# Kernel optimization log

Hardware: AMD Instinct MI355X
Metric: run time of the kernel (lower is better)

Reference implementation:

```python
import jax, jax.numpy as jnp
import numpy as np

R, N, F, H, C = 3, 100000, 256, 128, 2
N0, S1, D1, S2, D2 = 16384, 16384, 4096, 4096, 512


def setup_inputs() -> dict:
    key = jax.random.key(0)
    ks = jax.random.split(key, 13)
    return {
        "features": jax.random.normal(ks[0], (N, F), jnp.float32),
        "src_nodes": jax.random.randint(ks[1], (R, N0), 0, N),
        "dstsrc2src1": jax.random.randint(ks[2], (R, S1), 0, N0),
        "dstsrc2dst1": jax.random.randint(ks[3], (R, D1), 0, N0),
        "dif_mat1": jax.random.uniform(ks[4], (R, D1, S1), jnp.float32) / S1,
        "dstsrc2src2": jax.random.randint(ks[5], (R, S2), 0, D1),
        "dstsrc2dst2": jax.random.randint(ks[6], (R, D2), 0, D1),
        "dif_mat2": jax.random.uniform(ks[7], (R, D2, S2), jnp.float32) / S2,
        "w1": jax.random.normal(ks[8], (2 * F, H), jnp.float32) * 0.05,
        "w2": jax.random.normal(ks[9], (2 * H, H), jnp.float32) * 0.05,
        "relation_vectors": jax.random.uniform(ks[10], (R, H), jnp.float32),
        "attention_vec": jax.random.uniform(ks[11], (2 * H, 1), jnp.float32),
        "classifier_w": jax.random.normal(ks[12], (H, C), jnp.float32) * 0.05,
    }


def _agg(x, d2s, d2d, dif, w, rel_vec, att_vec):
    # x: [n, din]; dif: [d, s]; w: [2*din, H]
    agg = dif @ x[d2s]                                  # mean-diffused neighbor feats [d, din]
    h = jnp.concatenate([agg, x[d2d]], axis=1) @ w      # [d, H]
    rel = jnp.broadcast_to(rel_vec[None, :], (h.shape[0], rel_vec.shape[0]))
    score = (jnp.concatenate([h, rel], axis=1) @ att_vec)[:, 0]  # [d]
    att = jax.nn.softmax(score)                         # softmax over batch nodes
    return h * att[:, None]


def reference(features, src_nodes, dstsrc2src1, dstsrc2dst1, dif_mat1,
              dstsrc2src2, dstsrc2dst2, dif_mat2, w1, w2,
              relation_vectors, attention_vec, classifier_w):
    def per_relation(src, s1, d1, m1, s2, d2, m2, rel_vec):
        x = features[src]                               # gather node feats [N0, F]
        x = _agg(x, s1, d1, m1, w1, rel_vec, attention_vec)   # [D1, H]
        x = _agg(x, s2, d2, m2, w2, rel_vec, attention_vec)   # [D2, H]
        return x

    xs = jax.vmap(per_relation)(src_nodes, dstsrc2src1, dstsrc2dst1, dif_mat1,
                                dstsrc2src2, dstsrc2dst2, dif_mat2, relation_vectors)
    summed = jnp.sum(xs, axis=0)                        # sum over relations [D2, H]
    inv_norm = jax.lax.rsqrt(jnp.maximum(jnp.sum(summed * summed, axis=1, keepdims=True), 1e-12))
    normed = summed * inv_norm                          # tf.nn.l2_normalize(axis=1)
    return jax.nn.softmax(normed @ classifier_w, axis=-1)
```

## Files before the change

### kernel.cpp

```cpp
#include <hip/hip_runtime.h>
#include <hip/hip_bf16.h>
#include <math.h>

constexpr int Rc  = 3;
constexpr int Fc  = 256;
constexpr int Hc  = 128;
constexpr int N0c = 16384;
constexpr int S1c = 16384;
constexpr int D1c = 4096;
constexpr int S2c = 4096;
constexpr int D2c = 512;
constexpr int KH1 = 4;
constexpr int KH2 = 16;

typedef __bf16 bf16x8 __attribute__((ext_vector_type(8)));
typedef float  f32x4  __attribute__((ext_vector_type(4)));

__device__ __forceinline__ void glds16(const void* g, void* l) {
  __builtin_amdgcn_global_load_lds(
      (const __attribute__((address_space(1))) void*)g,
      (__attribute__((address_space(3))) void*)l, 16, 0, 0);
}

__device__ __forceinline__ bf16x8 cvt2(const float4 a, const float4 b) {
  bf16x8 c;
  c[0] = (__bf16)a.x; c[1] = (__bf16)a.y; c[2] = (__bf16)a.z; c[3] = (__bf16)a.w;
  c[4] = (__bf16)b.x; c[5] = (__bf16)b.y; c[6] = (__bf16)b.z; c[7] = (__bf16)b.w;
  return c;
}

__device__ __forceinline__ unsigned short bfbits(float v) {
  __bf16 b = (__bf16)v; unsigned short u;
  __builtin_memcpy(&u, &b, 2); return u;
}

__global__ __launch_bounds__(256, 2)
void wpack(const float* __restrict__ w1, const float* __restrict__ w2,
           unsigned char* __restrict__ wp) {
  const int tile = blockIdx.x, half = blockIdx.y, t = threadIdx.x;
  const float* src; int row0;
  if (tile < 4)       { src = w1; row0 = tile * 64; }
  else if (tile < 8)  { src = w1; row0 = 256 + (tile - 4) * 64; }
  else if (tile < 10) { src = w2; row0 = (tile - 8) * 64; }
  else                { src = w2; row0 = 128 + (tile - 10) * 64; }
  unsigned char* dst = wp + ((size_t)half * 12 + tile) * 16384;
  __shared__ float sm[64][132];
  {
    const int r = t >> 2, c0 = (t & 3) * 32;
#pragma unroll
    for (int j = 0; j < 8; j++)
      *(float4*)&sm[r][c0 + 4 * j] = *(const float4*)(src + (size_t)(row0 + r) * 128 + c0 + 4 * j);
  }
  __syncthreads();
  if (t < 128) {
    const int n = t;
#pragma unroll
    for (int ch = 0; ch < 8; ch++) {
      bf16x8 o;
#pragma unroll
      for (int e = 0; e < 8; e++) {
        float v = sm[ch * 8 + e][n];
        __bf16 h = (__bf16)v;
        o[e] = half ? (__bf16)(v - (float)h) : h;
      }
      *(bf16x8*)(dst + n * 128 + ((ch ^ (n & 7)) * 16)) = o;
    }
  }
}

__global__ __launch_bounds__(256, 3)
void gemm_gather(const float* __restrict__ Abase, int astride,
                 const int* __restrict__ srcn, const int* __restrict__ idx,
                 const float* __restrict__ scl,
                 const unsigned char* __restrict__ Bh,
                 const unsigned char* __restrict__ Bl,
                 float* __restrict__ Cf, unsigned char* __restrict__ Cp,
                 int rows, int K) {
  const int rel = blockIdx.y, s0 = blockIdx.x * 64;
  const int t = threadIdx.x, lane = t & 63, w = t >> 6;
  const int NT = K >> 6;
  const int mh = w >> 1, nh = w & 1;

  __shared__ __bf16 Asm[64 * 64];
  __shared__ __bf16 Bhs[128 * 64];
  __shared__ __bf16 Bls[128 * 64];

  const int arow = t >> 2, ak0 = (t & 3) * 16;
  const int row = s0 + arow;
  size_t arowg;
  if (idx) arowg = (size_t)srcn[rel * N0c + idx[(size_t)rel * rows + row]];
  else     arowg = (size_t)rel * rows + row;
  const float* aptr = Abase + arowg * astride + ak0;
  const float sc = scl ? scl[(size_t)rel * rows + row] : 1.0f;
  const int ac0 = ak0 >> 3;
  __bf16* asw0 = &Asm[arow * 64 + ((ac0    ) ^ (arow & 7)) * 8];
  __bf16* asw1 = &Asm[arow * 64 + ((ac0 + 1) ^ (arow & 7)) * 8];

  f32x4 acc[2][4] = {};

  for (int tl = 0; tl < NT; ++tl) {
    asm volatile("s_waitcnt lgkmcnt(0)" ::: "memory");
    __builtin_amdgcn_s_barrier();
    __builtin_amdgcn_sched_barrier(0);
    {
      const unsigned char* bh = Bh + (size_t)tl * 16384 + w * 4096 + lane * 16;
      const unsigned char* bl = Bl + (size_t)tl * 16384 + w * 4096 + lane * 16;
      char* dh = (char*)Bhs + w * 4096;
      char* dl = (char*)Bls + w * 4096;
#pragma unroll
      for (int i = 0; i < 4; i++) glds16(bh + i * 1024, dh + i * 1024);
#pragma unroll
      for (int i = 0; i < 4; i++) glds16(bl + i * 1024, dl + i * 1024);
    }
    {
      float4 a[4];
#pragma unroll
      for (int j = 0; j < 4; j++) a[j] = *(const float4*)(aptr + tl * 64 + 4 * j);
      if (scl) {
#pragma unroll
        for (int j = 0; j < 4; j++) { a[j].x *= sc; a[j].y *= sc; a[j].z *= sc; a[j].w *= sc; }
      }
      *(bf16x8*)asw0 = cvt2(a[0], a[1]);
      *(bf16x8*)asw1 = cvt2(a[2], a[3]);
    }
    asm volatile("s_waitcnt vmcnt(0) lgkmcnt(0)" ::: "memory");
    __builtin_amdgcn_s_barrier();
    __builtin_amdgcn_sched_barrier(0);
#pragma unroll
    for (int ks = 0; ks < 2; ks++) {
      const int ch = ks * 4 + (lane >> 4);
      bf16x8 af[2], bh[4], bl[4];
#pragma unroll
      for (int mi = 0; mi < 2; mi++) {
        int r = mh * 32 + mi * 16 + (lane & 15);
        af[mi] = *(const bf16x8*)&Asm[r * 64 + ((ch ^ (r & 7)) * 8)];
      }
#pragma unroll
      for (int ni = 0; ni < 4; ni++) {
        int n = nh * 64 + ni * 16 + (lane & 15);
        bh[ni] = *(const bf16x8*)&Bhs[n * 64 + ((ch ^ (n & 7)) * 8)];
        bl[ni] = *(const bf16x8*)&Bls[n * 64 + ((ch ^ (n & 7)) * 8)];
      }
#pragma unroll
      for (int mi = 0; mi < 2; mi++)
#pragma unroll
        for (int ni = 0; ni < 4; ni++) {
          acc[mi][ni] = __builtin_amdgcn_mfma_f32_16x16x32_bf16(af[mi], bh[ni], acc[mi][ni], 0, 0, 0);
          acc[mi][ni] = __builtin_amdgcn_mfma_f32_16x16x32_bf16(af[mi], bl[ni], acc[mi][ni], 0, 0, 0);
        }
    }
  }
  if (Cf) {
#pragma unroll
    for (int mi = 0; mi < 2; mi++)
#pragma unroll
      for (int ni = 0; ni < 4; ni++) {
        const int col = nh * 64 + ni * 16 + (lane & 15);
#pragma unroll
        for (int j = 0; j < 4; j++) {
          const int r = mh * 32 + mi * 16 + (lane >> 4) * 4 + j;
          Cf[((size_t)rel * rows + s0 + r) * 128 + col] = acc[mi][ni][j];
        }
      }
  } else {
    unsigned char* tile = Cp + ((size_t)(rel * (rows >> 6) + blockIdx.x)) * 16384;
#pragma unroll
    for (int mi = 0; mi < 2; mi++)
#pragma unroll
      for (int ni = 0; ni < 4; ni++) {
        const int sl0 = mh * 32 + mi * 16 + (lane >> 4) * 4;
        const int n = nh * 64 + ni * 16 + (lane & 15);
        const int ch = sl0 >> 3, e0 = sl0 & 7, cs = ch ^ (n & 7);
        ushort4 u;
        u.x = bfbits(acc[mi][ni][0]); u.y = bfbits(acc[mi][ni][1]);
        u.z = bfbits(acc[mi][ni][2]); u.w = bfbits(acc[mi][ni][3]);
        *(ushort4*)(tile + n * 128 + cs * 16 + e0 * 2) = u;
      }
  }
}

__global__ __launch_bounds__(256, 3)
void gemm_big(const float* __restrict__ A, const unsigned char* __restrict__ Bp,
              float* __restrict__ C, int M, int KTOT) {
  const int rel = blockIdx.z, kh = blockIdx.y;
  const int m0 = blockIdx.x * 64;
  const int t = threadIdx.x, lane = t & 63, w = t >> 6;
  const int KB = KTOT / gridDim.y, NT = KB >> 6;
  const int mh = w >> 1, nh = w & 1;

  const float* Ag = A + ((size_t)rel * M + m0) * KTOT + (size_t)kh * KB;
  const unsigned char* Bt = Bp + ((size_t)rel * (KTOT >> 6) + (size_t)kh * NT) * 16384;
  float* Cg = C + (((size_t)kh * Rc + rel) * M + m0) * 128;

  __shared__ __bf16 Asm[64 * 64];
  __shared__ __bf16 Bsm[2][128 * 64];

  f32x4 acc[2][4] = {};
  const int arow = t >> 2, ak0 = (t & 3) * 16;
  const float* aptr = Ag + (size_t)arow * KTOT + ak0;
  const int ac0 = ak0 >> 3;
  __bf16* asw0 = &Asm[arow * 64 + ((ac0    ) ^ (arow & 7)) * 8];
  __bf16* asw1 = &Asm[arow * 64 + ((ac0 + 1) ^ (arow & 7)) * 8];
  const unsigned char* bsrc = Bt + w * 4096 + lane * 16;

  float4 a0[4], a1[4];
#pragma unroll
  for (int j = 0; j < 4; j++) a0[j] = *(const float4*)(aptr + 4 * j);
  {
    char* bd = (char*)Bsm[0] + w * 4096;
#pragma unroll
    for (int i = 0; i < 4; i++) glds16(bsrc + i * 1024, bd + i * 1024);
  }

  for (int tl = 0; tl < NT; ++tl) {
    const int cur = tl & 1;
    asm volatile("s_waitcnt lgkmcnt(0)" ::: "memory");
    __builtin_amdgcn_s_barrier();
    __builtin_amdgcn_sched_barrier(0);
    if (tl + 1 < NT) {
      const unsigned char* bs = bsrc + (size_t)(tl + 1) * 16384;
      char* bd = (char*)Bsm[cur ^ 1] + w * 4096;
#pragma unroll
      for (int i = 0; i < 4; i++) glds16(bs + i * 1024, bd + i * 1024);
      const float* ap = aptr + (size_t)(tl + 1) * 64;
#pragma unroll
      for (int j = 0; j < 4; j++) a1[j] = *(const float4*)(ap + 4 * j);
    }
    *(bf16x8*)asw0 = cvt2(a0[0], a0[1]);
    *(bf16x8*)asw1 = cvt2(a0[2], a0[3]);
    if (tl + 1 < NT)
      asm volatile("s_waitcnt vmcnt(8) lgkmcnt(0)" ::: "memory");
    else
      asm volatile("s_waitcnt vmcnt(0) lgkmcnt(0)" ::: "memory");
    __builtin_amdgcn_s_barrier();
    __builtin_amdgcn_sched_barrier(0);
    const __bf16* Bc = Bsm[cur];
#pragma unroll
    for (int ks = 0; ks < 2; ks++) {
      const int ch = ks * 4 + (lane >> 4);
      bf16x8 af[2], bfr[4];
#pragma unroll
      for (int mi = 0; mi < 2; mi++) {
        int r = mh * 32 + mi * 16 + (lane & 15);
        af[mi] = *(const bf16x8*)&Asm[r * 64 + ((ch ^ (r & 7)) * 8)];
      }
#pragma unroll
      for (int ni = 0; ni < 4; ni++) {
        int n = nh * 64 + ni * 16 + (lane & 15);
        bfr[ni] = *(const bf16x8*)&Bc[n * 64 + ((ch ^ (n & 7)) * 8)];
      }
#pragma unroll
      for (int mi = 0; mi < 2; mi++)
#pragma unroll
        for (int ni = 0; ni < 4; ni++)
          acc[mi][ni] = __builtin_amdgcn_mfma_f32_16x16x32_bf16(af[mi], bfr[ni], acc[mi][ni], 0, 0, 0);
    }
#pragma unroll
    for (int j = 0; j < 4; j++) a0[j] = a1[j];
  }
#pragma unroll
  for (int mi = 0; mi < 2; mi++)
#pragma unroll
    for (int ni = 0; ni < 4; ni++) {
      const int col = nh * 64 + ni * 16 + (lane & 15);
#pragma unroll
      for (int j = 0; j < 4; j++) {
        const int r = mh * 32 + mi * 16 + (lane >> 4) * 4 + j;
        Cg[(size_t)r * 128 + col] = acc[mi][ni][j];
      }
    }
}

__global__ __launch_bounds__(256, 2)
void pgpack(const float* __restrict__ P, const int* __restrict__ d2s2,
            unsigned char* __restrict__ PGp) {
  const int rel = blockIdx.y, kb = blockIdx.x, t = threadIdx.x;
  __shared__ __bf16 sm[64][136];
  {
    const int kl = t >> 2, c0 = (t & 3) * 32;
    const int sr = d2s2[rel * S2c + kb * 64 + kl];
    const float4* p = (const float4*)(P + ((size_t)rel * D1c + sr) * 128 + c0);
#pragma unroll
    for (int j = 0; j < 4; j++)
      *(bf16x8*)&sm[kl][c0 + 8 * j] = cvt2(p[2 * j], p[2 * j + 1]);
  }
  __syncthreads();
  if (t < 128) {
    const int n = t;
    unsigned char* dst = PGp + ((size_t)(rel * (S2c >> 6) + kb)) * 16384;
#pragma unroll
    for (int ch = 0; ch < 8; ch++) {
      bf16x8 o;
#pragma unroll
      for (int e = 0; e < 8; e++) o[e] = sm[ch * 8 + e][n];
      *(bf16x8*)(dst + n * 128 + ((ch ^ (n & 7)) * 16)) = o;
    }
  }
}

__global__ __launch_bounds__(128, 4)
void combine1(const float* __restrict__ aggP, const float* __restrict__ xdw,
              const float* __restrict__ attv, float* __restrict__ h1,
              float* __restrict__ score1) {
  const int rel = blockIdx.y, d0 = blockIdx.x * 8, t = threadIdx.x;
  float acc[8];
#pragma unroll
  for (int i = 0; i < 8; i++) {
    const int d = d0 + i;
    float v = xdw[((size_t)rel * D1c + d) * 128 + t];
#pragma unroll
    for (int p = 0; p < KH1; p++)
      v += aggP[(((size_t)p * Rc + rel) * D1c + d) * 128 + t];
    acc[i] = v;
    h1[((size_t)rel * D1c + d) * 128 + t] = v;
  }
  const float avt = attv[t];
  __shared__ float sred[2][8];
#pragma unroll
  for (int i = 0; i < 8; i++) {
    float p = acc[i] * avt;
    p += __shfl_down(p, 32); p += __shfl_down(p, 16); p += __shfl_down(p, 8);
    p += __shfl_down(p, 4);  p += __shfl_down(p, 2);  p += __shfl_down(p, 1);
    if ((t & 63) == 0) sred[t >> 6][i] = p;
  }
  __syncthreads();
  if (t < 8) score1[rel * D1c + d0 + t] = sred[0][t] + sred[1][t];
}

__global__ __launch_bounds__(128, 4)
void combine2(const float* __restrict__ aggP2, const float* __restrict__ Q,
              const int* __restrict__ d2d2, const float* __restrict__ attv,
              float* __restrict__ h2, float* __restrict__ score2) {
  const int rel = blockIdx.y, d0 = blockIdx.x * 8, t = threadIdx.x;
  float acc[8];
#pragma unroll
  for (int i = 0; i < 8; i++) {
    const int d = d0 + i;
    const int qr = d2d2[rel * D2c + d];
    float v = Q[((size_t)rel * D1c + qr) * 128 + t];
#pragma unroll
    for (int p = 0; p < KH2; p++)
      v += aggP2[(((size_t)p * Rc + rel) * D2c + d) * 128 + t];
    acc[i] = v;
    h2[((size_t)rel * D2c + d) * 128 + t] = v;
  }
  const float avt = attv[t];
  __shared__ float sred[2][8];
#pragma unroll
  for (int i = 0; i < 8; i++) {
    float p = acc[i] * avt;
    p += __shfl_down(p, 32); p += __shfl_down(p, 16); p += __shfl_down(p, 8);
    p += __shfl_down(p, 4);  p += __shfl_down(p, 2);  p += __shfl_down(p, 1);
    if ((t & 63) == 0) sred[t >> 6][i] = p;
  }
  __syncthreads();
  if (t < 8) score2[rel * D2c + d0 + t] = sred[0][t] + sred[1][t];
}

__global__ __launch_bounds__(1024, 1)
void k4_softmax1(float* __restrict__ score1) {
  const int rel = blockIdx.x, t = threadIdx.x;
  float* s = score1 + rel * D1c;
  float v[4], m = -INFINITY;
#pragma unroll
  for (int j = 0; j < 4; j++) { v[j] = s[t + j * 1024]; m = fmaxf(m, v[j]); }
  __shared__ float red[1024];
  red[t] = m; __syncthreads();
  for (int off = 512; off > 0; off >>= 1) {
    if (t < off) red[t] = fmaxf(red[t], red[t + off]);
    __syncthreads();
  }
  const float M = red[0];
  __syncthreads();
  float e[4], sum = 0.f;
#pragma unroll
  for (int j = 0; j < 4; j++) { e[j] = expf(v[j] - M); sum += e[j]; }
  red[t] = sum; __syncthreads();
  for (int off = 512; off > 0; off >>= 1) {
    if (t < off) red[t] += red[t + off];
    __syncthreads();
  }
  const float inv = 1.0f / red[0];
#pragma unroll
  for (int j = 0; j < 4; j++) s[t + j * 1024] = e[j] * inv;
}

__global__ __launch_bounds__(512, 1)
void k8_softmax2(float* __restrict__ score2) {
  const int rel = blockIdx.x, t = threadIdx.x;
  float* s = score2 + rel * D2c;
  const float v = s[t];
  __shared__ float red[512];
  red[t] = v; __syncthreads();
  for (int off = 256; off > 0; off >>= 1) {
    if (t < off) red[t] = fmaxf(red[t], red[t + off]);
    __syncthreads();
  }
  const float M = red[0];
  __syncthreads();
  const float e = expf(v - M);
  red[t] = e; __syncthreads();
  for (int off = 256; off > 0; off >>= 1) {
    if (t < off) red[t] += red[t + off];
    __syncthreads();
  }
  s[t] = e / red[0];
}

__global__ __launch_bounds__(128, 4)
void k9_final(const float* __restrict__ h2, const float* __restrict__ att2,
              const float* __restrict__ cw, float* __restrict__ out) {
  const int d = blockIdx.x, t = threadIdx.x;
  float v = 0.f;
#pragma unroll
  for (int r = 0; r < Rc; r++)
    v += h2[((size_t)r * D2c + d) * Hc + t] * att2[r * D2c + d];
  float ss = v * v;
  ss += __shfl_down(ss, 32); ss += __shfl_down(ss, 16); ss += __shfl_down(ss, 8);
  ss += __shfl_down(ss, 4);  ss += __shfl_down(ss, 2);  ss += __shfl_down(ss, 1);
  __shared__ float sr[3][2];
  if ((t & 63) == 0) sr[0][t >> 6] = ss;
  __syncthreads();
  const float tot = sr[0][0] + sr[0][1];
  const float inv = rsqrtf(fmaxf(tot, 1e-12f));
  const float nv = v * inv;
  float p0 = nv * cw[t * 2], p1 = nv * cw[t * 2 + 1];
  p0 += __shfl_down(p0, 32); p0 += __shfl_down(p0, 16); p0 += __shfl_down(p0, 8);
  p0 += __shfl_down(p0, 4);  p0 += __shfl_down(p0, 2);  p0 += __shfl_down(p0, 1);
  p1 += __shfl_down(p1, 32); p1 += __shfl_down(p1, 16); p1 += __shfl_down(p1, 8);
  p1 += __shfl_down(p1, 4);  p1 += __shfl_down(p1, 2);  p1 += __shfl_down(p1, 1);
  if ((t & 63) == 0) { sr[1][t >> 6] = p0; sr[2][t >> 6] = p1; }
  __syncthreads();
  if (t == 0) {
    const float l0 = sr[1][0] + sr[1][1];
    const float l1 = sr[2][0] + sr[2][1];
    const float m = fmaxf(l0, l1);
    const float e0 = expf(l0 - m), e1 = expf(l1 - m);
    const float is = 1.0f / (e0 + e1);
    out[d * 2 + 0] = e0 * is;
    out[d * 2 + 1] = e1 * is;
  }
}

extern "C" void kernel_launch(void* const* d_in, const int* in_sizes, int n_in,
                              void* d_out, int out_size, void* d_ws, size_t ws_size,
                              hipStream_t stream) {
  (void)in_sizes; (void)n_in; (void)out_size; (void)ws_size;
  const float* feat = (const float*)d_in[0];
  const int*   srcn = (const int*)d_in[1];
  const int*   d2s1 = (const int*)d_in[2];
  const int*   d2d1 = (const int*)d_in[3];
  const float* dif1 = (const float*)d_in[4];
  const int*   d2s2 = (const int*)d_in[5];
  const int*   d2d2 = (const int*)d_in[6];
  const float* dif2 = (const float*)d_in[7];
  const float* w1   = (const float*)d_in[8];
  const float* w2   = (const float*)d_in[9];
  const float* attv = (const float*)d_in[11];
  const float* cw   = (const float*)d_in[12];
  float* out = (float*)d_out;

  char* p = (char*)d_ws;
  auto take = [&](size_t n) { char* r = p; p += (n + 255) & ~(size_t)255; return r; };
  unsigned char* wp   = (unsigned char*)take(24 * 16384);
  unsigned char* xgwp = (unsigned char*)take((size_t)Rc * 256 * 16384);
  float* xdw    = (float*)take((size_t)Rc * D1c * 128 * 4);
  float* aggP   = (float*)take((size_t)KH1 * Rc * D1c * 128 * 4);
  float* h1     = (float*)take((size_t)Rc * D1c * 128 * 4);
  float* score1 = (float*)take((size_t)Rc * D1c * 4);
  unsigned char* PGp = (unsigned char*)take((size_t)Rc * 64 * 16384);
  float* h2     = (float*)take((size_t)Rc * D2c * 128 * 4);
  float* score2 = (float*)take((size_t)Rc * D2c * 4);
  float* P = (float*)xgwp;
  float* Q = P + (size_t)Rc * D1c * 128;
  float* aggP2 = aggP;

  const unsigned char* w1t_h = wp;                const unsigned char* w1t_l = wp + 12 * 16384;
  const unsigned char* w1b_h = wp + 4 * 16384;    const unsigned char* w1b_l = wp + 16 * 16384;
  const unsigned char* w2P_h = wp + 8 * 16384;    const unsigned char* w2P_l = wp + 20 * 16384;
  const unsigned char* w2Q_h = wp + 10 * 16384;   const unsigned char* w2Q_l = wp + 22 * 16384;

  wpack<<<dim3(12, 2), 256, 0, stream>>>(w1, w2, wp);
  gemm_gather<<<dim3(S1c / 64, Rc), 256, 0, stream>>>(
      feat, Fc, srcn, d2s1, nullptr, w1t_h, w1t_l, nullptr, xgwp, S1c, 256);
  gemm_gather<<<dim3(D1c / 64, Rc), 256, 0, stream>>>(
      feat, Fc, srcn, d2d1, nullptr, w1b_h, w1b_l, xdw, nullptr, D1c, 256);
  gemm_big<<<dim3(D1c / 64, KH1, Rc), 256, 0, stream>>>(dif1, xgwp, aggP, D1c, S1c);
  combine1<<<dim3(D1c / 8, Rc), 128, 0, stream>>>(aggP, xdw, attv, h1, score1);
  k4_softmax1<<<Rc, 1024, 0, stream>>>(score1);
  gemm_gather<<<dim3(D1c / 64, Rc), 256, 0, stream>>>(
      h1, Hc, nullptr, nullptr, score1, w2P_h, w2P_l, P, nullptr, D1c, 128);
  gemm_gather<<<dim3(D1c / 64, Rc), 256, 0, stream>>>(
      h1, Hc, nullptr, nullptr, score1, w2Q_h, w2Q_l, Q, nullptr, D1c, 128);
  pgpack<<<dim3(S2c / 64, Rc), 256, 0, stream>>>(P, d2s2, PGp);
  gemm_big<<<dim3(D2c / 64, KH2, Rc), 256, 0, stream>>>(dif2, PGp, aggP2, D2c, S2c);
  combine2<<<dim3(D2c / 8, Rc), 128, 0, stream>>>(aggP2, Q, d2d2, attv, h2, score2);
  k8_softmax2<<<Rc, 512, 0, stream>>>(score2);
  k9_final<<<D2c, 128, 0, stream>>>(h2, score2, cw, out);
}
```

Baseline: 299.8 us.

## Merge gather-GEMM launches and add XCD-aware block swizzle for big GEMM

Two layer-1 gather GEMM launches are merged into one grid with a job split on blockIdx.x. The two layer-2 P/Q GEMMs are merged via blockIdx.z. Both kernels are specialised with compile-time K and no null-pointer branches. The layer-1 big GEMM now uses a 1D grid whose block index is remapped so blocks sharing the same B tiles (rel, kh) land on the same XCD, aiming for better L2 reuse. This cuts launch count and tail effects, at the cost of duplicated kernel code.

```diff
diff --git a/kernel.cpp b/kernel.cpp
--- a/kernel.cpp
+++ b/kernel.cpp
@@ -69,16 +69,22 @@
 }
 
 __global__ __launch_bounds__(256, 3)
-void gemm_gather(const float* __restrict__ Abase, int astride,
-                 const int* __restrict__ srcn, const int* __restrict__ idx,
-                 const float* __restrict__ scl,
-                 const unsigned char* __restrict__ Bh,
-                 const unsigned char* __restrict__ Bl,
-                 float* __restrict__ Cf, unsigned char* __restrict__ Cp,
-                 int rows, int K) {
-  const int rel = blockIdx.y, s0 = blockIdx.x * 64;
+void gg_layer1(const float* __restrict__ feat, const int* __restrict__ srcn,
+               const int* __restrict__ d2s1, const int* __restrict__ d2d1,
+               const unsigned char* __restrict__ wp,
+               unsigned char* __restrict__ xgwp, float* __restrict__ xdw) {
+  const int rel = blockIdx.y;
+  int bx = blockIdx.x;
+  const int job = bx >= 256 ? 1 : 0;
+  if (job) bx -= 256;
+  const int s0 = bx * 64;
+  const int rows = job ? D1c : S1c;
+  const int* idx = job ? d2d1 : d2s1;
+  const unsigned char* Bh = wp + (size_t)(job ? 4 : 0) * 16384;
+  const unsigned char* Bl = wp + (size_t)(12 + (job ? 4 : 0)) * 16384;
+
   const int t = threadIdx.x, lane = t & 63, w = t >> 6;
-  const int NT = K >> 6;
+  const int NT = 4;
   const int mh = w >> 1, nh = w & 1;
 
   __shared__ __bf16 Asm[64 * 64];
@@ -87,11 +93,8 @@
 
   const int arow = t >> 2, ak0 = (t & 3) * 16;
   const int row = s0 + arow;
-  size_t arowg;
-  if (idx) arowg = (size_t)srcn[rel * N0c + idx[(size_t)rel * rows + row]];
-  else     arowg = (size_t)rel * rows + row;
-  const float* aptr = Abase + arowg * astride + ak0;
-  const float sc = scl ? scl[(size_t)rel * rows + row] : 1.0f;
+  const size_t arowg = (size_t)srcn[rel * N0c + idx[(size_t)rel * rows + row]];
+  const float* aptr = feat + arowg * Fc + ak0;
   const int ac0 = ak0 >> 3;
   __bf16* asw0 = &Asm[arow * 64 + ((ac0    ) ^ (arow & 7)) * 8];
   __bf16* asw1 = &Asm[arow * 64 + ((ac0 + 1) ^ (arow & 7)) * 8];
@@ -116,10 +119,6 @@
       float4 a[4];
 #pragma unroll
       for (int j = 0; j < 4; j++) a[j] = *(const float4*)(aptr + tl * 64 + 4 * j);
-      if (scl) {
-#pragma unroll
-        for (int j = 0; j < 4; j++) { a[j].x *= sc; a[j].y *= sc; a[j].z *= sc; a[j].w *= sc; }
-      }
       *(bf16x8*)asw0 = cvt2(a[0], a[1]);
       *(bf16x8*)asw1 = cvt2(a[2], a[3]);
     }
@@ -150,7 +149,7 @@
         }
     }
   }
-  if (Cf) {
+  if (job) {
 #pragma unroll
     for (int mi = 0; mi < 2; mi++)
 #pragma unroll
@@ -159,11 +158,11 @@
 #pragma unroll
         for (int j = 0; j < 4; j++) {
           const int r = mh * 32 + mi * 16 + (lane >> 4) * 4 + j;
-          Cf[((size_t)rel * rows + s0 + r) * 128 + col] = acc[mi][ni][j];
+          xdw[((size_t)rel * D1c + s0 + r) * 128 + col] = acc[mi][ni][j];
         }
       }
   } else {
-    unsigned char* tile = Cp + ((size_t)(rel * (rows >> 6) + blockIdx.x)) * 16384;
+    unsigned char* tile = xgwp + ((size_t)(rel * (S1c >> 6) + bx)) * 16384;
 #pragma unroll
     for (int mi = 0; mi < 2; mi++)
 #pragma unroll
@@ -180,12 +179,113 @@
 }
 
 __global__ __launch_bounds__(256, 3)
+void gg_layer2(const float* __restrict__ h1, const float* __restrict__ scl,
+               const unsigned char* __restrict__ wp,
+               float* __restrict__ P, float* __restrict__ Q) {
+  const int rel = blockIdx.y, s0 = blockIdx.x * 64, z = blockIdx.z;
+  const unsigned char* Bh = wp + (size_t)(z ? 10 : 8) * 16384;
+  const unsigned char* Bl = wp + (size_t)(z ? 22 : 20) * 16384;
+  float* Cf = z ? Q : P;
+
+  const int t = threadIdx.x, lane = t & 63, w = t >> 6;
+  const int NT = 2;
+  const int mh = w >> 1, nh = w & 1;
+
+  __shared__ __bf16 Asm[64 * 64];
+  __shared__ __bf16 Bhs[128 * 64];
+  __shared__ __bf16 Bls[128 * 64];
+
+  const int arow = t >> 2, ak0 = (t & 3) * 16;
+  const int row = s0 + arow;
+  const float* aptr = h1 + ((size_t)rel * D1c + row) * Hc + ak0;
+  const float sc = scl[(size_t)rel * D1c + row];
+  const int ac0 = ak0 >> 3;
+  __bf16* asw0 = &Asm[arow * 64 + ((ac0    ) ^ (arow & 7)) * 8];
+  __bf16* asw1 = &Asm[arow * 64 + ((ac0 + 1) ^ (arow & 7)) * 8];
+
+  f32x4 acc[2][4] = {};
+
+  for (int tl = 0; tl < NT; ++tl) {
+    asm volatile("s_waitcnt lgkmcnt(0)" ::: "memory");
+    __builtin_amdgcn_s_barrier();
+    __builtin_amdgcn_sched_barrier(0);
+    {
+      const unsigned char* bh = Bh + (size_t)tl * 16384 + w * 4096 + lane * 16;
+      const unsigned char* bl = Bl + (size_t)tl * 16384 + w * 4096 + lane * 16;
+      char* dh = (char*)Bhs + w * 4096;
+      char* dl = (char*)Bls + w * 4096;
+#pragma unroll
+      for (int i = 0; i < 4; i++) glds16(bh + i * 1024, dh + i * 1024);
+#pragma unroll
+      for (int i = 0; i < 4; i++) glds16(bl + i * 1024, dl + i * 1024);
+    }
+    {
+      float4 a[4];
+#pragma unroll
+      for (int j = 0; j < 4; j++) a[j] = *(const float4*)(aptr + tl * 64 + 4 * j);
+#pragma unroll
+      for (int j = 0; j < 4; j++) { a[j].x *= sc; a[j].y *= sc; a[j].z *= sc; a[j].w *= sc; }
+      *(bf16x8*)asw0 = cvt2(a[0], a[1]);
+      *(bf16x8*)asw1 = cvt2(a[2], a[3]);
+    }
+    asm volatile("s_waitcnt vmcnt(0) lgkmcnt(0)" ::: "memory");
+    __builtin_amdgcn_s_barrier();
+    __builtin_amdgcn_sched_barrier(0);
+#pragma unroll
+    for (int ks = 0; ks < 2; ks++) {
+      const int ch = ks * 4 + (lane >> 4);
+      bf16x8 af[2], bh[4], bl[4];
+#pragma unroll
+      for (int mi = 0; mi < 2; mi++) {
+        int r = mh * 32 + mi * 16 + (lane & 15);
+        af[mi] = *(const bf16x8*)&Asm[r * 64 + ((ch ^ (r & 7)) * 8)];
+      }
+#pragma unroll
+      for (int ni = 0; ni < 4; ni++) {
+        int n = nh * 64 + ni * 16 + (lane & 15);
+        bh[ni] = *(const bf16x8*)&Bhs[n * 64 + ((ch ^ (n & 7)) * 8)];
+        bl[ni] = *(const bf16x8*)&Bls[n * 64 + ((ch ^ (n & 7)) * 8)];
+      }
+#pragma unroll
+      for (int mi = 0; mi < 2; mi++)
+#pragma unroll
+        for (int ni = 0; ni < 4; ni++) {
+          acc[mi][ni] = __builtin_amdgcn_mfma_f32_16x16x32_bf16(af[mi], bh[ni], acc[mi][ni], 0, 0, 0);
+          acc[mi][ni] = __builtin_amdgcn_mfma_f32_16x16x32_bf16(af[mi], bl[ni], acc[mi][ni], 0, 0, 0);
+        }
+    }
+  }
+#pragma unroll
+  for (int mi = 0; mi < 2; mi++)
+#pragma unroll
+    for (int ni = 0; ni < 4; ni++) {
+      const int col = nh * 64 + ni * 16 + (lane & 15);
+#pragma unroll
+      for (int j = 0; j < 4; j++) {
+        const int r = mh * 32 + mi * 16 + (lane >> 4) * 4 + j;
+        Cf[((size_t)rel * D1c + s0 + r) * 128 + col] = acc[mi][ni][j];
+      }
+    }
+}
+
+template <int SWZ>
+__global__ __launch_bounds__(256, 3)
 void gemm_big(const float* __restrict__ A, const unsigned char* __restrict__ Bp,
-              float* __restrict__ C, int M, int KTOT) {
-  const int rel = blockIdx.z, kh = blockIdx.y;
-  const int m0 = blockIdx.x * 64;
+              float* __restrict__ C, int M, int KTOT, int KH) {
+  int rel, kh, m0;
+  if (SWZ) {
+    const int F = blockIdx.x;
+    const int xcd = F & 7, r = F >> 3;
+    const int sub = r >> 5, m = r & 31;
+    const int h = xcd + 8 * sub;
+    const int g = h >> 1;
+    rel = g >> 2; kh = g & 3;
+    m0 = ((h & 1) * 32 + m) * 64;
+  } else {
+    rel = blockIdx.z; kh = blockIdx.y; m0 = blockIdx.x * 64;
+  }
   const int t = threadIdx.x, lane = t & 63, w = t >> 6;
-  const int KB = KTOT / gridDim.y, NT = KB >> 6;
+  const int KB = KTOT / KH, NT = KB >> 6;
   const int mh = w >> 1, nh = w & 1;
 
   const float* Ag = A + ((size_t)rel * M + m0) * KTOT + (size_t)kh * KB;
@@ -475,25 +575,14 @@
   float* Q = P + (size_t)Rc * D1c * 128;
   float* aggP2 = aggP;
 
-  const unsigned char* w1t_h = wp;                const unsigned char* w1t_l = wp + 12 * 16384;
-  const unsigned char* w1b_h = wp + 4 * 16384;    const unsigned char* w1b_l = wp + 16 * 16384;
-  const unsigned char* w2P_h = wp + 8 * 16384;    const unsigned char* w2P_l = wp + 20 * 16384;
-  const unsigned char* w2Q_h = wp + 10 * 16384;   const unsigned char* w2Q_l = wp + 22 * 16384;
-
   wpack<<<dim3(12, 2), 256, 0, stream>>>(w1, w2, wp);
-  gemm_gather<<<dim3(S1c / 64, Rc), 256, 0, stream>>>(
-      feat, Fc, srcn, d2s1, nullptr, w1t_h, w1t_l, nullptr, xgwp, S1c, 256);
-  gemm_gather<<<dim3(D1c / 64, Rc), 256, 0, stream>>>(
-      feat, Fc, srcn, d2d1, nullptr, w1b_h, w1b_l, xdw, nullptr, D1c, 256);
-  gemm_big<<<dim3(D1c / 64, KH1, Rc), 256, 0, stream>>>(dif1, xgwp, aggP, D1c, S1c);
+  gg_layer1<<<dim3(320, Rc), 256, 0, stream>>>(feat, srcn, d2s1, d2d1, wp, xgwp, xdw);
+  gemm_big<1><<<768, 256, 0, stream>>>(dif1, xgwp, aggP, D1c, S1c, KH1);
   combine1<<<dim3(D1c / 8, Rc), 128, 0, stream>>>(aggP, xdw, attv, h1, score1);
   k4_softmax1<<<Rc, 1024, 0, stream>>>(score1);
-  gemm_gather<<<dim3(D1c / 64, Rc), 256, 0, stream>>>(
-      h1, Hc, nullptr, nullptr, score1, w2P_h, w2P_l, P, nullptr, D1c, 128);
-  gemm_gather<<<dim3(D1c / 64, Rc), 256, 0, stream>>>(
-      h1, Hc, nullptr, nullptr, score1, w2Q_h, w2Q_l, Q, nullptr, D1c, 128);
+  gg_layer2<<<dim3(D1c / 64, Rc, 2), 256, 0, stream>>>(h1, score1, wp, P, Q);
   pgpack<<<dim3(S2c / 64, Rc), 256, 0, stream>>>(P, d2s2, PGp);
-  gemm_big<<<dim3(D2c / 64, KH2, Rc), 256, 0, stream>>>(dif2, PGp, aggP2, D2c, S2c);
+  gemm_big<0><<<dim3(D2c / 64, KH2, Rc), 256, 0, stream>>>(dif2, PGp, aggP2, D2c, S2c, KH2);
   combine2<<<dim3(D2c / 8, Rc), 128, 0, stream>>>(aggP2, Q, d2d2, attv, h2, score2);
   k8_softmax2<<<Rc, 512, 0, stream>>>(score2);
   k9_final<<<D2c, 128, 0, stream>>>(h2, score2, cw, out);
```

New measurement: 285.0 us. 4.9% less time.
